# Optimization experiments

Measured on AMD Instinct MI355X. Metric: run time of the kernel, lower is better.

Reference implementation:

```python
import jax, jax.numpy as jnp
import numpy as np

B, C, D, H, W = 4, 64, 16, 32, 32
K = 1024  # num_embeddings


def setup_inputs() -> dict:
    key = jax.random.key(0)
    k1, k2 = jax.random.split(key)
    z_e = jax.random.normal(k1, (B, C, D, H, W), dtype=jnp.float32)
    embedding = jax.random.normal(k2, (K, C), dtype=jnp.float32)
    return {"z_e": z_e, "embedding": embedding}


def reference(z_e, embedding):
    Bb, Cc, Dd, Hh, Ww = z_e.shape
    # (B, D, H, W, C) -> (N, C)
    flat = jnp.transpose(z_e, (0, 2, 3, 4, 1)).reshape(-1, Cc)
    # squared-euclidean distances to codebook: [N, K]
    distances = (
        jnp.sum(flat * flat, axis=1, keepdims=True)
        - 2.0 * flat @ embedding.T
        + jnp.sum(embedding * embedding, axis=1)
    )
    encoding_indices = jnp.argmin(distances, axis=1)  # [N]
    # one_hot @ embedding == gather (same math, efficient form)
    quantized_flat = embedding[encoding_indices]  # [N, C]
    quantized = jnp.transpose(
        quantized_flat.reshape(Bb, Dd, Hh, Ww, Cc), (0, 4, 1, 2, 3)
    )
    commitment_loss = jnp.mean((jax.lax.stop_gradient(quantized) - z_e) ** 2)
    codebook_loss = jnp.mean((quantized - jax.lax.stop_gradient(z_e)) ** 2)
    # straight-through estimator
    quantized_st = z_e + jax.lax.stop_gradient(quantized - z_e)
    indices = encoding_indices.reshape(Bb, Dd, Hh, Ww)
    return quantized_st, codebook_loss, commitment_loss, indices
```

## Files before the change

kernel.cpp:

```cpp
#include <hip/hip_runtime.h>

#define NPOS    65536
#define CDIM    64
#define KCODES  1024
#define NCHUNK  4
#define KCHUNK  256
#define SPATIAL 16384
#define QELEMS  4194304

#define NORM_OFF   0
#define PSCORE_OFF 1024
#define PIDX_OFF   (1024 + NPOS * NCHUNK)
#define LOSS_OFF   (1024 + 2 * NPOS * NCHUNK)

__global__ void k_norms(const float* __restrict__ emb, float* __restrict__ wsf) {
    int k = blockIdx.x * blockDim.x + threadIdx.x;
    if (k == 0) wsf[LOSS_OFF] = 0.0f;
    if (k < KCODES) {
        const float4* e4 = (const float4*)(emb + (size_t)k * CDIM);
        float s = 0.0f;
#pragma unroll
        for (int c = 0; c < CDIM / 4; ++c) {
            float4 e = e4[c];
            s += e.x * e.x + e.y * e.y + e.z * e.z + e.w * e.w;
        }
        wsf[NORM_OFF + k] = s;
    }
}

__global__ __launch_bounds__(256, 4) void k_search(const float* __restrict__ z_e,
                                                   const float* __restrict__ emb,
                                                   float* __restrict__ wsf) {
    const int bp  = blockIdx.x >> 2;
    const int bk  = blockIdx.x & 3;
    const int n   = bp * 256 + threadIdx.x;
    const int b   = n >> 14;
    const int dhw = n & (SPATIAL - 1);

    const float* zb = z_e + ((size_t)b * CDIM) * SPATIAL + dhw;
    float x[CDIM];
#pragma unroll
    for (int c = 0; c < CDIM; ++c) x[c] = zb[(size_t)c * SPATIAL];

    const int   kbase = bk * KCHUNK;
    const float* __restrict__ ep = emb + (size_t)kbase * CDIM;
    const float* __restrict__ nrm = wsf + NORM_OFF + kbase;

    float best = 3.4e38f;
    int   bidx = kbase;
    for (int k = 0; k < KCHUNK; ++k) {
        const float4* e4 = (const float4*)(ep + (size_t)k * CDIM);
        float s0 = 0.f, s1 = 0.f, s2 = 0.f, s3 = 0.f;
#pragma unroll
        for (int c = 0; c < CDIM / 4; ++c) {
            float4 e = e4[c];
            s0 = fmaf(x[4 * c + 0], e.x, s0);
            s1 = fmaf(x[4 * c + 1], e.y, s1);
            s2 = fmaf(x[4 * c + 2], e.z, s2);
            s3 = fmaf(x[4 * c + 3], e.w, s3);
        }
        float dot   = (s0 + s1) + (s2 + s3);
        float score = fmaf(-2.0f, dot, nrm[k]);
        if (score < best) { best = score; bidx = kbase + k; }
    }
    wsf[PSCORE_OFF + bk * NPOS + n]          = best;
    ((int*)wsf)[PIDX_OFF + bk * NPOS + n]    = bidx;
}

__global__ void k_finalize(const float* __restrict__ z_e,
                           const float* __restrict__ emb,
                           float* __restrict__ out,
                           float* __restrict__ wsf) {
    const int n   = blockIdx.x * 256 + threadIdx.x;
    const int b   = n >> 14;
    const int dhw = n & (SPATIAL - 1);

    float best = wsf[PSCORE_OFF + n];
    int   bidx = ((const int*)wsf)[PIDX_OFF + n];
#pragma unroll
    for (int ch = 1; ch < NCHUNK; ++ch) {
        float s = wsf[PSCORE_OFF + ch * NPOS + n];
        int   i = ((const int*)wsf)[PIDX_OFF + ch * NPOS + n];
        if (s < best) { best = s; bidx = i; }
    }

    out[QELEMS + 2 + n] = (float)bidx;

    const float*  zb = z_e + ((size_t)b * CDIM) * SPATIAL + dhw;
    float*        qb = out + ((size_t)b * CDIM) * SPATIAL + dhw;
    const float4* e4 = (const float4*)(emb + (size_t)bidx * CDIM);

    float lsum = 0.0f;
#pragma unroll
    for (int c4 = 0; c4 < CDIM / 4; ++c4) {
        float4 ev = e4[c4];
        float  evs[4] = {ev.x, ev.y, ev.z, ev.w};
#pragma unroll
        for (int j = 0; j < 4; ++j) {
            int   c  = 4 * c4 + j;
            float xv = zb[(size_t)c * SPATIAL];
            float d  = evs[j] - xv;
            qb[(size_t)c * SPATIAL] = xv + d;
            lsum = fmaf(d, d, lsum);
        }
    }

#pragma unroll
    for (int off = 32; off > 0; off >>= 1) lsum += __shfl_down(lsum, off);
    if ((threadIdx.x & 63) == 0) atomicAdd(&wsf[LOSS_OFF], lsum);
}

__global__ void k_loss(const float* __restrict__ wsf, float* __restrict__ out) {
    float m = wsf[LOSS_OFF] / (float)QELEMS;
    out[QELEMS]     = m;
    out[QELEMS + 1] = m;
}

extern "C" void kernel_launch(void* const* d_in, const int* in_sizes, int n_in,
                              void* d_out, int out_size, void* d_ws, size_t ws_size,
                              hipStream_t stream) {
    const float* z_e = (const float*)d_in[0];
    const float* emb = (const float*)d_in[1];
    float*       out = (float*)d_out;
    float*       wsf = (float*)d_ws;

    k_norms<<<KCODES / 256, 256, 0, stream>>>(emb, wsf);
    k_search<<<(NPOS / 256) * NCHUNK, 256, 0, stream>>>(z_e, emb, wsf);
    k_finalize<<<NPOS / 256, 256, 0, stream>>>(z_e, emb, out, wsf);
    k_loss<<<1, 1, 0, stream>>>(wsf, out);
}
```

Measured before the change: 239.1 us.

## Fuse norm computation into search and reduce chunks via packed 64-bit atomicMin

Computes codebook norms per block into shared memory, removing the separate norms kernel. Partial argmin results across codebook chunks are combined with a 64-bit atomicMin on a packed (monotonic score, index) key instead of storing partial arrays and reducing them in finalize. Codebook chunking changes from 4×256 to 8×128 with a higher occupancy hint and unroll 2. This doubles the per-position z_e loads across chunks and adds per-block norm recomputation plus a workspace memset.

Result: no change. 238.1 us (-0.4%).

```diff
diff --git a/kernel.cpp b/kernel.cpp
--- a/kernel.cpp
+++ b/kernel.cpp
@@ -3,51 +3,49 @@
 #define NPOS    65536
 #define CDIM    64
 #define KCODES  1024
-#define NCHUNK  4
-#define KCHUNK  256
+#define NCHUNK  8
+#define KCHUNK  128
 #define SPATIAL 16384
 #define QELEMS  4194304
 
-#define NORM_OFF   0
-#define PSCORE_OFF 1024
-#define PIDX_OFF   (1024 + NPOS * NCHUNK)
-#define LOSS_OFF   (1024 + 2 * NPOS * NCHUNK)
+#define LOSSF_IDX 131072
 
-__global__ void k_norms(const float* __restrict__ emb, float* __restrict__ wsf) {
-    int k = blockIdx.x * blockDim.x + threadIdx.x;
-    if (k == 0) wsf[LOSS_OFF] = 0.0f;
-    if (k < KCODES) {
-        const float4* e4 = (const float4*)(emb + (size_t)k * CDIM);
+__global__ __launch_bounds__(256, 6) void k_search(const float* __restrict__ z_e,
+                                                   const float* __restrict__ emb,
+                                                   unsigned long long* __restrict__ wsu,
+                                                   float* __restrict__ wsf) {
+    __shared__ float nrm[KCHUNK];
+    const int bp    = blockIdx.x >> 3;
+    const int bk    = blockIdx.x & 7;
+    const int kbase = bk * KCHUNK;
+
+    if (threadIdx.x < KCHUNK) {
+        const float4* e4 = (const float4*)(emb + (size_t)(kbase + threadIdx.x) * CDIM);
         float s = 0.0f;
 #pragma unroll
         for (int c = 0; c < CDIM / 4; ++c) {
             float4 e = e4[c];
             s += e.x * e.x + e.y * e.y + e.z * e.z + e.w * e.w;
         }
-        wsf[NORM_OFF + k] = s;
+        nrm[threadIdx.x] = s;
     }
-}
+    if (blockIdx.x == 0 && threadIdx.x == 0) wsf[LOSSF_IDX] = 0.0f;
+    __syncthreads();
 
-__global__ __launch_bounds__(256, 4) void k_search(const float* __restrict__ z_e,
-                                                   const float* __restrict__ emb,
-                                                   float* __restrict__ wsf) {
-    const int bp  = blockIdx.x >> 2;
-    const int bk  = blockIdx.x & 3;
     const int n   = bp * 256 + threadIdx.x;
     const int b   = n >> 14;
     const int dhw = n & (SPATIAL - 1);
 
-    const float* zb = z_e + ((size_t)b * CDIM) * SPATIAL + dhw;
+    const float* zb = z_e + (size_t)b * (CDIM * SPATIAL) + dhw;
     float x[CDIM];
 #pragma unroll
     for (int c = 0; c < CDIM; ++c) x[c] = zb[(size_t)c * SPATIAL];
 
-    const int   kbase = bk * KCHUNK;
     const float* __restrict__ ep = emb + (size_t)kbase * CDIM;
-    const float* __restrict__ nrm = wsf + NORM_OFF + kbase;
 
     float best = 3.4e38f;
-    int   bidx = kbase;
+    int   bidx = 0;
+#pragma unroll 2
     for (int k = 0; k < KCHUNK; ++k) {
         const float4* e4 = (const float4*)(ep + (size_t)k * CDIM);
         float s0 = 0.f, s1 = 0.f, s2 = 0.f, s3 = 0.f;
@@ -61,33 +59,29 @@
         }
         float dot   = (s0 + s1) + (s2 + s3);
         float score = fmaf(-2.0f, dot, nrm[k]);
-        if (score < best) { best = score; bidx = kbase + k; }
+        if (score < best) { best = score; bidx = k; }
     }
-    wsf[PSCORE_OFF + bk * NPOS + n]          = best;
-    ((int*)wsf)[PIDX_OFF + bk * NPOS + n]    = bidx;
+
+    unsigned u    = __float_as_uint(best);
+    unsigned mono = (u & 0x80000000u) ? ~u : (u | 0x80000000u);
+    unsigned long long packed = ((unsigned long long)mono << 10) | (unsigned)(kbase + bidx);
+    atomicMin(&wsu[n], packed);
 }
 
 __global__ void k_finalize(const float* __restrict__ z_e,
                            const float* __restrict__ emb,
                            float* __restrict__ out,
+                           const unsigned long long* __restrict__ wsu,
                            float* __restrict__ wsf) {
-    const int n   = blockIdx.x * 256 + threadIdx.x;
-    const int b   = n >> 14;
-    const int dhw = n & (SPATIAL - 1);
-
-    float best = wsf[PSCORE_OFF + n];
-    int   bidx = ((const int*)wsf)[PIDX_OFF + n];
-#pragma unroll
-    for (int ch = 1; ch < NCHUNK; ++ch) {
-        float s = wsf[PSCORE_OFF + ch * NPOS + n];
-        int   i = ((const int*)wsf)[PIDX_OFF + ch * NPOS + n];
-        if (s < best) { best = s; bidx = i; }
-    }
+    const int n    = blockIdx.x * 256 + threadIdx.x;
+    const int b    = n >> 14;
+    const int dhw  = n & (SPATIAL - 1);
+    const int bidx = (int)(wsu[n] & 1023ull);
 
     out[QELEMS + 2 + n] = (float)bidx;
 
-    const float*  zb = z_e + ((size_t)b * CDIM) * SPATIAL + dhw;
-    float*        qb = out + ((size_t)b * CDIM) * SPATIAL + dhw;
+    const float*  zb = z_e + (size_t)b * (CDIM * SPATIAL) + dhw;
+    float*        qb = out + (size_t)b * (CDIM * SPATIAL) + dhw;
     const float4* e4 = (const float4*)(emb + (size_t)bidx * CDIM);
 
     float lsum = 0.0f;
@@ -107,11 +101,11 @@
 
 #pragma unroll
     for (int off = 32; off > 0; off >>= 1) lsum += __shfl_down(lsum, off);
-    if ((threadIdx.x & 63) == 0) atomicAdd(&wsf[LOSS_OFF], lsum);
+    if ((threadIdx.x & 63) == 0) atomicAdd(&wsf[LOSSF_IDX], lsum);
 }
 
 __global__ void k_loss(const float* __restrict__ wsf, float* __restrict__ out) {
-    float m = wsf[LOSS_OFF] / (float)QELEMS;
+    float m = wsf[LOSSF_IDX] / (float)QELEMS;
     out[QELEMS]     = m;
     out[QELEMS + 1] = m;
 }
@@ -122,10 +116,12 @@
     const float* z_e = (const float*)d_in[0];
     const float* emb = (const float*)d_in[1];
     float*       out = (float*)d_out;
+    unsigned long long* wsu = (unsigned long long*)d_ws;
     float*       wsf = (float*)d_ws;
 
-    k_norms<<<KCODES / 256, 256, 0, stream>>>(emb, wsf);
-    k_search<<<(NPOS / 256) * NCHUNK, 256, 0, stream>>>(z_e, emb, wsf);
-    k_finalize<<<NPOS / 256, 256, 0, stream>>>(z_e, emb, out, wsf);
+    hipMemsetAsync(d_ws, 0xFF, (size_t)NPOS * 8, stream);
+
+    k_search<<<(NPOS / 256) * NCHUNK, 256, 0, stream>>>(z_e, emb, wsu, wsf);
+    k_finalize<<<NPOS / 256, 256, 0, stream>>>(z_e, emb, out, wsu, wsf);
     k_loss<<<1, 1, 0, stream>>>(wsf, out);
 }
```
